# Optimization experiments

Hardware: AMD Instinct MI355X
Metric: run time of the kernel (lower is better)

Reference implementation:

```python
import jax, jax.numpy as jnp
import numpy as np

EMBED = 256
HEADS = 8
LEVELS = 1
POINTS = 4
HEAD_DIM = EMBED // HEADS  # 32
SPATIAL = [(200, 200)]     # static (H, W) per level
BS = 2
NQ = 40000
NV = sum(h * w for h, w in SPATIAL)


def setup_inputs() -> dict:
    key = jax.random.key(0)
    ks = jax.random.split(key, 12)
    s = 0.02
    inp = {
        "query": jax.random.normal(ks[0], (BS, NQ, EMBED), jnp.float32),
        "value": jax.random.normal(ks[1], (BS, NV, EMBED), jnp.float32),
        "reference_points": jax.random.uniform(ks[2], (BS, NQ, LEVELS, 2), jnp.float32),
        "spatial_shapes": jnp.array(SPATIAL, dtype=jnp.int32),
        "W_value": jax.random.normal(ks[3], (EMBED, EMBED), jnp.float32) * s,
        "b_value": jax.random.normal(ks[4], (EMBED,), jnp.float32) * s,
        "W_off": jax.random.normal(ks[5], (EMBED, HEADS * LEVELS * POINTS * 2), jnp.float32) * s,
        "b_off": jax.random.normal(ks[6], (HEADS * LEVELS * POINTS * 2,), jnp.float32) * s,
        "W_attn": jax.random.normal(ks[7], (EMBED, HEADS * LEVELS * POINTS), jnp.float32) * s,
        "b_attn": jax.random.normal(ks[8], (HEADS * LEVELS * POINTS,), jnp.float32) * s,
        "W_out": jax.random.normal(ks[9], (EMBED, EMBED), jnp.float32) * s,
        "b_out": jax.random.normal(ks[10], (EMBED,), jnp.float32) * s,
    }
    return inp


def _bilinear_sample(v_l, x, y, H, W):
    """grid_sample(bilinear, padding zeros, align_corners=False) on flat spatial.
    v_l: [bs, heads, H*W, d]; x, y: [bs, nq, heads, P] pixel coords.
    Returns [bs, nq, heads, P, d]."""
    bs = v_l.shape[0]
    nq = x.shape[1]
    x0 = jnp.floor(x)
    y0 = jnp.floor(y)
    out = jnp.zeros((bs, nq, HEADS, POINTS, HEAD_DIM), v_l.dtype)
    for dx in (0, 1):
        for dy in (0, 1):
            xi = x0 + dx
            yi = y0 + dy
            w = (1.0 - jnp.abs(x - xi)) * (1.0 - jnp.abs(y - yi))
            valid = (xi >= 0) & (xi <= W - 1) & (yi >= 0) & (yi <= H - 1)
            xi_c = jnp.clip(xi, 0, W - 1).astype(jnp.int32)
            yi_c = jnp.clip(yi, 0, H - 1).astype(jnp.int32)
            idx = yi_c * W + xi_c                               # [bs,nq,heads,P]
            idx = idx.transpose(0, 2, 1, 3).reshape(bs, HEADS, nq * POINTS)
            g = jnp.take_along_axis(v_l, idx[..., None], axis=2)  # [bs,heads,nq*P,d]
            g = g.reshape(bs, HEADS, nq, POINTS, HEAD_DIM).transpose(0, 2, 1, 3, 4)
            out = out + g * (w * valid.astype(w.dtype))[..., None]
    return out


def reference(query, value, reference_points, spatial_shapes,
              W_value, b_value, W_off, b_off, W_attn, b_attn, W_out, b_out):
    bs, nq, _ = query.shape
    # value projection
    v = (value @ W_value + b_value).reshape(bs, -1, HEADS, HEAD_DIM)
    v = v.transpose(0, 2, 1, 3)  # [bs, heads, nv, d]
    # sampling offsets and attention weights from query
    off = (query @ W_off + b_off).reshape(bs, nq, HEADS, LEVELS, POINTS, 2)
    aw = (query @ W_attn + b_attn).reshape(bs, nq, HEADS, LEVELS * POINTS)
    aw = jax.nn.softmax(aw, axis=-1).reshape(bs, nq, HEADS, LEVELS, POINTS)
    # sampling locations in [0,1] (reference_points last dim == 2 branch)
    normalizer = jnp.stack([spatial_shapes[:, 1], spatial_shapes[:, 0]], -1).astype(query.dtype)  # [L,2]=(W,H)
    loc = reference_points[:, :, None, :, None, :] + off / normalizer[None, None, None, :, None, :]
    out = jnp.zeros((bs, nq, HEADS, HEAD_DIM), query.dtype)
    start = 0
    for lvl, (H, W) in enumerate(SPATIAL):
        v_l = v[:, :, start:start + H * W]            # [bs,heads,HW,d]
        g = 2.0 * loc[:, :, :, lvl] - 1.0             # [bs,nq,heads,P,2] in [-1,1]
        px = ((g[..., 0] + 1.0) * W - 1.0) / 2.0      # align_corners=False
        py = ((g[..., 1] + 1.0) * H - 1.0) / 2.0
        sampled = _bilinear_sample(v_l, px, py, H, W)  # [bs,nq,heads,P,d]
        out = out + (sampled * aw[:, :, :, lvl, :, None]).sum(axis=3)
        start += H * W
    out = out.reshape(bs, nq, EMBED) @ W_out + b_out
    # dropout is identity in eval; identity residual = query (no query_pos)
    return out + query
```

## Files before the change

kernel.cpp:

```cpp
#include <hip/hip_runtime.h>


typedef float  f4  __attribute__((ext_vector_type(4)));
typedef float  fx4 __attribute__((ext_vector_type(4)));
typedef short  s8  __attribute__((ext_vector_type(8)));
typedef short  s4  __attribute__((ext_vector_type(4)));

#define KDIM    256
#define NVPIX   40000
#define GH      200
#define GW      200
#define LDP     68

__device__ __forceinline__ short f2bf(float f) {
  union { float f; unsigned u; } v; v.f = f;
  unsigned r = v.u + 0x7fffu + ((v.u >> 16) & 1u);
  return (short)(r >> 16);
}
__device__ __forceinline__ float bf2f(unsigned short h) {
  union { unsigned u; float f; } v; v.u = ((unsigned)h) << 16; return v.f;
}

__global__ void prep_k(const float* __restrict__ Wv, const float* __restrict__ Wo,
                       const float* __restrict__ Woff, const float* __restrict__ Wattn,
                       const float* __restrict__ boff, const float* __restrict__ battn,
                       unsigned short* __restrict__ Wv_t, unsigned short* __restrict__ Wo_t,
                       unsigned short* __restrict__ Wp_t, float* __restrict__ bp)
{
  int i = blockIdx.x * 256 + threadIdx.x;
  if (i < 65536) {
    int n = i >> 8, k = i & 255;
    Wv_t[i] = (unsigned short)f2bf(Wv[k * 256 + n]);
  } else if (i < 131072) {
    int j = i - 65536; int n = j >> 8, k = j & 255;
    Wo_t[j] = (unsigned short)f2bf(Wo[k * 256 + n]);
  } else if (i < 163840) {
    int j = i - 131072; int n = j >> 8, k = j & 255;
    float val = (n < 64) ? Woff[k * 64 + n] : ((n < 96) ? Wattn[k * 32 + (n - 64)] : 0.f);
    Wp_t[j] = (unsigned short)f2bf(val);
  } else if (i < 163968) {
    int j = i - 163840;
    bp[j] = (j < 64) ? boff[j] : ((j < 96) ? battn[j - 64] : 0.f);
  }
}

template<int ABF, int CBF, int RES>
__global__ __launch_bounds__(256)
void gemm_k(const void* __restrict__ Ap, const unsigned short* __restrict__ Bt,
            const float* __restrict__ bias, const float* __restrict__ resid,
            void* __restrict__ Cp, int N)
{
  __shared__ short As[128 * LDP];
  __shared__ short Bs[128 * LDP];
  const int t  = threadIdx.x;
  const int m0 = blockIdx.x * 128;
  const int n0 = blockIdx.y * 128;
  const int lane = t & 63;
  const int w  = t >> 6;
  const int wm = (w >> 1) * 64;
  const int wn = (w & 1) * 64;
  const int fr = lane & 15;
  const int quad = lane >> 4;

  fx4 acc[4][4];
  #pragma unroll
  for (int i = 0; i < 4; i++)
    #pragma unroll
    for (int j = 0; j < 4; j++) { fx4 z = {0.f, 0.f, 0.f, 0.f}; acc[i][j] = z; }

  f4 pa[8];
  s8 pa8[4];
  s8 pb[4];

  auto loadA = [&](int k0) {
    if (ABF) {
      const unsigned short* base = (const unsigned short*)Ap + (size_t)m0 * KDIM + k0;
      #pragma unroll
      for (int j = 0; j < 4; j++) {
        int id = t + j * 256;
        int row = id >> 3, kp = (id & 7) * 8;
        pa8[j] = *(const s8*)(base + (size_t)row * KDIM + kp);
      }
    } else {
      const float* base = (const float*)Ap + (size_t)m0 * KDIM + k0;
      #pragma unroll
      for (int j = 0; j < 8; j++) {
        int id = t + j * 256;
        int row = id >> 4, kp = (id & 15) * 4;
        pa[j] = *(const f4*)(base + (size_t)row * KDIM + kp);
      }
    }
  };
  auto loadB = [&](int k0) {
    const unsigned short* base = Bt + (size_t)n0 * KDIM + k0;
    #pragma unroll
    for (int j = 0; j < 4; j++) {
      int id = t + j * 256;
      int row = id >> 3, kp = (id & 7) * 8;
      pb[j] = *(const s8*)(base + (size_t)row * KDIM + kp);
    }
  };
  auto storeAB = [&]() {
    if (ABF) {
      #pragma unroll
      for (int j = 0; j < 4; j++) {
        int id = t + j * 256;
        int row = id >> 3, kp = (id & 7) * 8;
        *(s8*)(&As[row * LDP + kp]) = pa8[j];
      }
    } else {
      #pragma unroll
      for (int j = 0; j < 8; j++) {
        int id = t + j * 256;
        int row = id >> 4, kp = (id & 15) * 4;
        s4 c;
        #pragma unroll
        for (int e = 0; e < 4; e++) c[e] = f2bf(pa[j][e]);
        *(s4*)(&As[row * LDP + kp]) = c;
      }
    }
    #pragma unroll
    for (int j = 0; j < 4; j++) {
      int id = t + j * 256;
      int row = id >> 3, kp = (id & 7) * 8;
      *(s8*)(&Bs[row * LDP + kp]) = pb[j];
    }
  };

  loadA(0); loadB(0);
  #pragma unroll
  for (int it = 0; it < 4; ++it) {
    __syncthreads();
    storeAB();
    __syncthreads();
    if (it < 3) { loadA((it + 1) * 64); loadB((it + 1) * 64); }
    #pragma unroll
    for (int kk = 0; kk < 2; kk++) {
      s8 afr[4], bfr[4];
      #pragma unroll
      for (int i = 0; i < 4; i++)
        afr[i] = *(const s8*)(&As[(wm + i * 16 + fr) * LDP + kk * 32 + quad * 8]);
      #pragma unroll
      for (int i = 0; i < 4; i++)
        bfr[i] = *(const s8*)(&Bs[(wn + i * 16 + fr) * LDP + kk * 32 + quad * 8]);
      #pragma unroll
      for (int i = 0; i < 4; i++)
        #pragma unroll
        for (int j = 0; j < 4; j++)
          acc[i][j] = __builtin_amdgcn_mfma_f32_16x16x32_bf16(afr[i], bfr[j], acc[i][j], 0, 0, 0);
    }
  }

  #pragma unroll
  for (int i = 0; i < 4; i++) {
    const int mbase = m0 + wm + i * 16 + quad * 4;
    #pragma unroll
    for (int j = 0; j < 4; j++) {
      const int n = n0 + wn + j * 16 + fr;
      const float bn = bias[n];
      #pragma unroll
      for (int r = 0; r < 4; r++) {
        const size_t m = (size_t)(mbase + r);
        float v = acc[i][j][r] + bn;
        if (RES) v += resid[m * (size_t)N + n];
        if (CBF) ((unsigned short*)Cp)[m * (size_t)N + n] = (unsigned short)f2bf(v);
        else     ((float*)Cp)[m * (size_t)N + n] = v;
      }
    }
  }
}

__global__ __launch_bounds__(256)
void sample_k(const unsigned short* __restrict__ v, const float* __restrict__ p,
              const float* __restrict__ ref, unsigned short* __restrict__ o)
{
  const int t  = threadIdx.x;
  const int q0 = blockIdx.x * 8;
  __shared__ float sp[8][128];
  __shared__ float sref[16];
  {
    const float* pb = p + (size_t)q0 * 128;
    #pragma unroll
    for (int j = 0; j < 4; j++) {
      int i = t + j * 256;
      sp[i >> 7][i & 127] = pb[i];
    }
    if (t < 16) sref[t] = ref[(size_t)q0 * 2 + t];
  }
  __syncthreads();

  const int qi = t >> 5;
  const int h  = (t >> 2) & 7;
  const int dg = t & 3;
  const int q  = q0 + qi;
  const int b  = (q >= 40000) ? 1 : 0;

  const float lg0 = sp[qi][64 + h * 4 + 0], lg1 = sp[qi][64 + h * 4 + 1];
  const float lg2 = sp[qi][64 + h * 4 + 2], lg3 = sp[qi][64 + h * 4 + 3];
  const float mx = fmaxf(fmaxf(lg0, lg1), fmaxf(lg2, lg3));
  const float e0 = __expf(lg0 - mx), e1 = __expf(lg1 - mx);
  const float e2 = __expf(lg2 - mx), e3 = __expf(lg3 - mx);
  const float inv = 1.f / (e0 + e1 + e2 + e3);
  const float aws[4] = {e0 * inv, e1 * inv, e2 * inv, e3 * inv};
  const float rx = sref[qi * 2], ry = sref[qi * 2 + 1];

  const unsigned short* vb = v + (size_t)b * NVPIX * 256;
  const int cbase = h * 32 + dg * 8;

  float acc[8];
  #pragma unroll
  for (int e = 0; e < 8; e++) acc[e] = 0.f;

  #pragma unroll
  for (int pt = 0; pt < 4; ++pt) {
    const float ox = sp[qi][h * 8 + pt * 2], oy = sp[qi][h * 8 + pt * 2 + 1];
    const float px = rx * 200.f + ox - 0.5f;
    const float py = ry * 200.f + oy - 0.5f;
    const float x0f = floorf(px), y0f = floorf(py);
    const int ix = (int)x0f, iy = (int)y0f;
    const float fx = px - x0f, fy = py - y0f;
    const float a = aws[pt];
    const float vx0 = (ix >= 0 && ix < GW) ? 1.f : 0.f;
    const float vx1 = (ix + 1 >= 0 && ix + 1 < GW) ? 1.f : 0.f;
    const float vy0 = (iy >= 0 && iy < GH) ? 1.f : 0.f;
    const float vy1 = (iy + 1 >= 0 && iy + 1 < GH) ? 1.f : 0.f;
    const float w00 = a * (1.f - fx) * (1.f - fy) * vx0 * vy0;
    const float w01 = a * fx * (1.f - fy) * vx1 * vy0;
    const float w10 = a * (1.f - fx) * fy * vx0 * vy1;
    const float w11 = a * fx * fy * vx1 * vy1;
    const int ix0c = min(max(ix, 0), GW - 1);
    const int ix1c = min(max(ix + 1, 0), GW - 1);
    const int iy0c = min(max(iy, 0), GH - 1);
    const int iy1c = min(max(iy + 1, 0), GH - 1);
    const int r0 = iy0c * (GW * 256) + cbase;
    const int r1 = iy1c * (GW * 256) + cbase;
    s8 g00 = *(const s8*)(vb + r0 + ix0c * 256);
    s8 g01 = *(const s8*)(vb + r0 + ix1c * 256);
    s8 g10 = *(const s8*)(vb + r1 + ix0c * 256);
    s8 g11 = *(const s8*)(vb + r1 + ix1c * 256);
    #pragma unroll
    for (int e = 0; e < 8; e++) {
      acc[e] += w00 * bf2f((unsigned short)g00[e]) + w01 * bf2f((unsigned short)g01[e])
              + w10 * bf2f((unsigned short)g10[e]) + w11 * bf2f((unsigned short)g11[e]);
    }
  }

  s8 res;
  #pragma unroll
  for (int e = 0; e < 8; e++) res[e] = f2bf(acc[e]);
  *(s8*)(o + (size_t)q * 256 + cbase) = res;
}

extern "C" void kernel_launch(void* const* d_in, const int* in_sizes, int n_in,
                              void* d_out, int out_size, void* d_ws, size_t ws_size,
                              hipStream_t stream)
{
  const float* query = (const float*)d_in[0];
  const float* value = (const float*)d_in[1];
  const float* refp  = (const float*)d_in[2];
  const float* Wv    = (const float*)d_in[4];
  const float* bv    = (const float*)d_in[5];
  const float* Woff  = (const float*)d_in[6];
  const float* boff  = (const float*)d_in[7];
  const float* Wattn = (const float*)d_in[8];
  const float* battn = (const float*)d_in[9];
  const float* Wo    = (const float*)d_in[10];
  const float* bo    = (const float*)d_in[11];

  char* ws = (char*)d_ws;
  unsigned short* ws_v = (unsigned short*)ws;
  float*          ws_p = (float*)(ws + 40960000);
  unsigned short* ws_o = (unsigned short*)(ws + 81920000);
  unsigned short* Wv_t = (unsigned short*)(ws + 122880000);
  unsigned short* Wo_t = Wv_t + 65536;
  unsigned short* Wp_t = Wo_t + 65536;
  float*          bp   = (float*)(Wp_t + 32768);

  hipLaunchKernelGGL(prep_k, dim3(641), dim3(256), 0, stream,
                     Wv, Wo, Woff, Wattn, boff, battn, Wv_t, Wo_t, Wp_t, bp);
  hipLaunchKernelGGL((gemm_k<0, 1, 0>), dim3(625, 2), dim3(256), 0, stream,
                     (const void*)value, Wv_t, bv, (const float*)nullptr, (void*)ws_v, 256);
  hipLaunchKernelGGL((gemm_k<0, 0, 0>), dim3(625, 1), dim3(256), 0, stream,
                     (const void*)query, Wp_t, bp, (const float*)nullptr, (void*)ws_p, 128);
  hipLaunchKernelGGL(sample_k, dim3(10000), dim3(256), 0, stream,
                     ws_v, ws_p, refp, ws_o);
  hipLaunchKernelGGL((gemm_k<1, 0, 1>), dim3(625, 2), dim3(256), 0, stream,
                     (const void*)ws_o, Wo_t, bo, query, (void*)d_out, 256);
}
```

Measured before the change: 353.5 us.

## Fuse bilinear sampling with output projection GEMM and residual add

Merges the sampling kernel and the final output-projection GEMM into one kernel. Each block samples 64 queries (one thread per query-head computing all 32 channels) into shared memory in bf16, then runs an MFMA GEMM against Wo_t and adds bias plus the query residual. This removes the round trip of the sampled intermediate through global memory and one launch. In exchange each thread holds more registers (32 accumulators plus 16 MFMA accumulators), gathers are no longer spread across 4 threads per head, and only 1250 blocks are launched, which may lower occupancy and latency hiding.

```diff
diff --git a/kernel.cpp b/kernel.cpp
--- a/kernel.cpp
+++ b/kernel.cpp
@@ -11,6 +11,8 @@
 #define GH      200
 #define GW      200
 #define LDP     68
+#define SMPP    264
+#define BSP     36
 
 __device__ __forceinline__ short f2bf(float f) {
   union { float f; unsigned u; } v; v.f = f;
@@ -44,11 +46,10 @@
   }
 }
 
-template<int ABF, int CBF, int RES>
+template<int CBF>
 __global__ __launch_bounds__(256)
-void gemm_k(const void* __restrict__ Ap, const unsigned short* __restrict__ Bt,
-            const float* __restrict__ bias, const float* __restrict__ resid,
-            void* __restrict__ Cp, int N)
+void gemm_k(const float* __restrict__ Ap, const unsigned short* __restrict__ Bt,
+            const float* __restrict__ bias, void* __restrict__ Cp, int N)
 {
   __shared__ short As[128 * LDP];
   __shared__ short Bs[128 * LDP];
@@ -69,26 +70,15 @@
     for (int j = 0; j < 4; j++) { fx4 z = {0.f, 0.f, 0.f, 0.f}; acc[i][j] = z; }
 
   f4 pa[8];
-  s8 pa8[4];
   s8 pb[4];
 
   auto loadA = [&](int k0) {
-    if (ABF) {
-      const unsigned short* base = (const unsigned short*)Ap + (size_t)m0 * KDIM + k0;
-      #pragma unroll
-      for (int j = 0; j < 4; j++) {
-        int id = t + j * 256;
-        int row = id >> 3, kp = (id & 7) * 8;
-        pa8[j] = *(const s8*)(base + (size_t)row * KDIM + kp);
-      }
-    } else {
-      const float* base = (const float*)Ap + (size_t)m0 * KDIM + k0;
-      #pragma unroll
-      for (int j = 0; j < 8; j++) {
-        int id = t + j * 256;
-        int row = id >> 4, kp = (id & 15) * 4;
-        pa[j] = *(const f4*)(base + (size_t)row * KDIM + kp);
-      }
+    const float* base = Ap + (size_t)m0 * KDIM + k0;
+    #pragma unroll
+    for (int j = 0; j < 8; j++) {
+      int id = t + j * 256;
+      int row = id >> 4, kp = (id & 15) * 4;
+      pa[j] = *(const f4*)(base + (size_t)row * KDIM + kp);
     }
   };
   auto loadB = [&](int k0) {
@@ -101,23 +91,14 @@
     }
   };
   auto storeAB = [&]() {
-    if (ABF) {
-      #pragma unroll
-      for (int j = 0; j < 4; j++) {
-        int id = t + j * 256;
-        int row = id >> 3, kp = (id & 7) * 8;
-        *(s8*)(&As[row * LDP + kp]) = pa8[j];
-      }
-    } else {
-      #pragma unroll
-      for (int j = 0; j < 8; j++) {
-        int id = t + j * 256;
-        int row = id >> 4, kp = (id & 15) * 4;
-        s4 c;
-        #pragma unroll
-        for (int e = 0; e < 4; e++) c[e] = f2bf(pa[j][e]);
-        *(s4*)(&As[row * LDP + kp]) = c;
-      }
+    #pragma unroll
+    for (int j = 0; j < 8; j++) {
+      int id = t + j * 256;
+      int row = id >> 4, kp = (id & 15) * 4;
+      s4 c;
+      #pragma unroll
+      for (int e = 0; e < 4; e++) c[e] = f2bf(pa[j][e]);
+      *(s4*)(&As[row * LDP + kp]) = c;
     }
     #pragma unroll
     for (int j = 0; j < 4; j++) {
@@ -162,7 +143,6 @@
       for (int r = 0; r < 4; r++) {
         const size_t m = (size_t)(mbase + r);
         float v = acc[i][j][r] + bn;
-        if (RES) v += resid[m * (size_t)N + n];
         if (CBF) ((unsigned short*)Cp)[m * (size_t)N + n] = (unsigned short)f2bf(v);
         else     ((float*)Cp)[m * (size_t)N + n] = v;
       }
@@ -171,84 +151,143 @@
 }
 
 __global__ __launch_bounds__(256)
-void sample_k(const unsigned short* __restrict__ v, const float* __restrict__ p,
-              const float* __restrict__ ref, unsigned short* __restrict__ o)
+void fused_k(const unsigned short* __restrict__ v, const float* __restrict__ p,
+             const float* __restrict__ ref, const unsigned short* __restrict__ Wo_t,
+             const float* __restrict__ bo, const float* __restrict__ query,
+             float* __restrict__ out)
 {
+  __shared__ short smp[64 * SMPP];
+  __shared__ short Bs[256 * BSP];
   const int t  = threadIdx.x;
-  const int q0 = blockIdx.x * 8;
-  __shared__ float sp[8][128];
-  __shared__ float sref[16];
-  {
-    const float* pb = p + (size_t)q0 * 128;
-    #pragma unroll
-    for (int j = 0; j < 4; j++) {
-      int i = t + j * 256;
-      sp[i >> 7][i & 127] = pb[i];
-    }
-    if (t < 16) sref[t] = ref[(size_t)q0 * 2 + t];
-  }
-  __syncthreads();
-
-  const int qi = t >> 5;
-  const int h  = (t >> 2) & 7;
-  const int dg = t & 3;
-  const int q  = q0 + qi;
-  const int b  = (q >= 40000) ? 1 : 0;
-
-  const float lg0 = sp[qi][64 + h * 4 + 0], lg1 = sp[qi][64 + h * 4 + 1];
-  const float lg2 = sp[qi][64 + h * 4 + 2], lg3 = sp[qi][64 + h * 4 + 3];
-  const float mx = fmaxf(fmaxf(lg0, lg1), fmaxf(lg2, lg3));
-  const float e0 = __expf(lg0 - mx), e1 = __expf(lg1 - mx);
-  const float e2 = __expf(lg2 - mx), e3 = __expf(lg3 - mx);
-  const float inv = 1.f / (e0 + e1 + e2 + e3);
-  const float aws[4] = {e0 * inv, e1 * inv, e2 * inv, e3 * inv};
-  const float rx = sref[qi * 2], ry = sref[qi * 2 + 1];
-
-  const unsigned short* vb = v + (size_t)b * NVPIX * 256;
-  const int cbase = h * 32 + dg * 8;
-
-  float acc[8];
-  #pragma unroll
-  for (int e = 0; e < 8; e++) acc[e] = 0.f;
-
-  #pragma unroll
-  for (int pt = 0; pt < 4; ++pt) {
-    const float ox = sp[qi][h * 8 + pt * 2], oy = sp[qi][h * 8 + pt * 2 + 1];
-    const float px = rx * 200.f + ox - 0.5f;
-    const float py = ry * 200.f + oy - 0.5f;
-    const float x0f = floorf(px), y0f = floorf(py);
-    const int ix = (int)x0f, iy = (int)y0f;
-    const float fx = px - x0f, fy = py - y0f;
-    const float a = aws[pt];
-    const float vx0 = (ix >= 0 && ix < GW) ? 1.f : 0.f;
-    const float vx1 = (ix + 1 >= 0 && ix + 1 < GW) ? 1.f : 0.f;
-    const float vy0 = (iy >= 0 && iy < GH) ? 1.f : 0.f;
-    const float vy1 = (iy + 1 >= 0 && iy + 1 < GH) ? 1.f : 0.f;
-    const float w00 = a * (1.f - fx) * (1.f - fy) * vx0 * vy0;
-    const float w01 = a * fx * (1.f - fy) * vx1 * vy0;
-    const float w10 = a * (1.f - fx) * fy * vx0 * vy1;
-    const float w11 = a * fx * fy * vx1 * vy1;
-    const int ix0c = min(max(ix, 0), GW - 1);
-    const int ix1c = min(max(ix + 1, 0), GW - 1);
-    const int iy0c = min(max(iy, 0), GH - 1);
-    const int iy1c = min(max(iy + 1, 0), GH - 1);
-    const int r0 = iy0c * (GW * 256) + cbase;
-    const int r1 = iy1c * (GW * 256) + cbase;
-    s8 g00 = *(const s8*)(vb + r0 + ix0c * 256);
-    s8 g01 = *(const s8*)(vb + r0 + ix1c * 256);
-    s8 g10 = *(const s8*)(vb + r1 + ix0c * 256);
-    s8 g11 = *(const s8*)(vb + r1 + ix1c * 256);
-    #pragma unroll
-    for (int e = 0; e < 8; e++) {
-      acc[e] += w00 * bf2f((unsigned short)g00[e]) + w01 * bf2f((unsigned short)g01[e])
-              + w10 * bf2f((unsigned short)g10[e]) + w11 * bf2f((unsigned short)g11[e]);
-    }
-  }
-
-  s8 res;
-  #pragma unroll
-  for (int e = 0; e < 8; e++) res[e] = f2bf(acc[e]);
-  *(s8*)(o + (size_t)q * 256 + cbase) = res;
+  const int q0 = blockIdx.x * 64;
+
+  #pragma unroll
+  for (int itA = 0; itA < 2; ++itA) {
+    const int id = t + itA * 256;
+    const int qi = id >> 3;
+    const int h  = id & 7;
+    const int q  = q0 + qi;
+    const int b  = (q >= 40000) ? 1 : 0;
+    const float* pq = p + (size_t)q * 128;
+    const f4 off0 = *(const f4*)(pq + h * 8);
+    const f4 off1 = *(const f4*)(pq + h * 8 + 4);
+    const f4 lg   = *(const f4*)(pq + 64 + h * 4);
+    const float rx = ref[(size_t)q * 2], ry = ref[(size_t)q * 2 + 1];
+
+    const float mx = fmaxf(fmaxf(lg[0], lg[1]), fmaxf(lg[2], lg[3]));
+    const float e0 = __expf(lg[0] - mx), e1 = __expf(lg[1] - mx);
+    const float e2 = __expf(lg[2] - mx), e3 = __expf(lg[3] - mx);
+    const float inv = 1.f / (e0 + e1 + e2 + e3);
+    const float aws[4] = {e0 * inv, e1 * inv, e2 * inv, e3 * inv};
+    const float offs[8] = {off0[0], off0[1], off0[2], off0[3],
+                           off1[0], off1[1], off1[2], off1[3]};
+
+    const unsigned short* vb = v + (size_t)b * NVPIX * 256 + h * 32;
+
+    float acc[32];
+    #pragma unroll
+    for (int e = 0; e < 32; e++) acc[e] = 0.f;
+
+    #pragma unroll
+    for (int pt = 0; pt < 4; ++pt) {
+      const float px = rx * 200.f + offs[pt * 2]     - 0.5f;
+      const float py = ry * 200.f + offs[pt * 2 + 1] - 0.5f;
+      const float x0f = floorf(px), y0f = floorf(py);
+      const int ix = (int)x0f, iy = (int)y0f;
+      const float fx = px - x0f, fy = py - y0f;
+      const float a = aws[pt];
+      const float vx0 = (ix >= 0 && ix < GW) ? 1.f : 0.f;
+      const float vx1 = (ix + 1 >= 0 && ix + 1 < GW) ? 1.f : 0.f;
+      const float vy0 = (iy >= 0 && iy < GH) ? 1.f : 0.f;
+      const float vy1 = (iy + 1 >= 0 && iy + 1 < GH) ? 1.f : 0.f;
+      const float w00 = a * (1.f - fx) * (1.f - fy) * vx0 * vy0;
+      const float w01 = a * fx * (1.f - fy) * vx1 * vy0;
+      const float w10 = a * (1.f - fx) * fy * vx0 * vy1;
+      const float w11 = a * fx * fy * vx1 * vy1;
+      const int ix0c = min(max(ix, 0), GW - 1);
+      const int ix1c = min(max(ix + 1, 0), GW - 1);
+      const int iy0c = min(max(iy, 0), GH - 1);
+      const int iy1c = min(max(iy + 1, 0), GH - 1);
+      const unsigned short* c00 = vb + ((long)iy0c * GW + ix0c) * 256;
+      const unsigned short* c01 = vb + ((long)iy0c * GW + ix1c) * 256;
+      const unsigned short* c10 = vb + ((long)iy1c * GW + ix0c) * 256;
+      const unsigned short* c11 = vb + ((long)iy1c * GW + ix1c) * 256;
+      #pragma unroll
+      for (int g = 0; g < 4; g++) {
+        s8 g00 = *(const s8*)(c00 + g * 8);
+        s8 g01 = *(const s8*)(c01 + g * 8);
+        s8 g10 = *(const s8*)(c10 + g * 8);
+        s8 g11 = *(const s8*)(c11 + g * 8);
+        #pragma unroll
+        for (int e = 0; e < 8; e++) {
+          acc[g * 8 + e] += w00 * bf2f((unsigned short)g00[e])
+                          + w01 * bf2f((unsigned short)g01[e])
+                          + w10 * bf2f((unsigned short)g10[e])
+                          + w11 * bf2f((unsigned short)g11[e]);
+        }
+      }
+    }
+    #pragma unroll
+    for (int g = 0; g < 4; g++) {
+      s8 res;
+      #pragma unroll
+      for (int e = 0; e < 8; e++) res[e] = f2bf(acc[g * 8 + e]);
+      *(s8*)(&smp[qi * SMPP + h * 32 + g * 8]) = res;
+    }
+  }
+
+  const int lane = t & 63;
+  const int w    = t >> 6;
+  const int fr   = lane & 15;
+  const int quad = lane >> 4;
+
+  fx4 oacc[16];
+  #pragma unroll
+  for (int j = 0; j < 16; j++) { fx4 z = {0.f, 0.f, 0.f, 0.f}; oacc[j] = z; }
+
+  s8 pbB[4];
+  auto loadB = [&](int k0) {
+    #pragma unroll
+    for (int j = 0; j < 4; j++) {
+      int id = t + j * 256;
+      int row = id >> 2, kg = id & 3;
+      pbB[j] = *(const s8*)(Wo_t + (size_t)row * KDIM + k0 + kg * 8);
+    }
+  };
+  auto storeB = [&]() {
+    #pragma unroll
+    for (int j = 0; j < 4; j++) {
+      int id = t + j * 256;
+      int row = id >> 2, kg = id & 3;
+      *(s8*)(&Bs[row * BSP + kg * 8]) = pbB[j];
+    }
+  };
+
+  loadB(0);
+  #pragma unroll
+  for (int it = 0; it < 8; ++it) {
+    storeB();
+    __syncthreads();
+    if (it < 7) loadB((it + 1) * 32);
+    const s8 afr = *(const s8*)(&smp[(w * 16 + fr) * SMPP + it * 32 + quad * 8]);
+    #pragma unroll
+    for (int j = 0; j < 16; j++) {
+      const s8 bfr = *(const s8*)(&Bs[(j * 16 + fr) * BSP + quad * 8]);
+      oacc[j] = __builtin_amdgcn_mfma_f32_16x16x32_bf16(afr, bfr, oacc[j], 0, 0, 0);
+    }
+    if (it < 7) __syncthreads();
+  }
+
+  #pragma unroll
+  for (int j = 0; j < 16; j++) {
+    const int n = j * 16 + fr;
+    const float bn = bo[n];
+    #pragma unroll
+    for (int r = 0; r < 4; r++) {
+      const size_t m = (size_t)(q0 + w * 16 + quad * 4 + r);
+      out[m * 256 + n] = oacc[j][r] + bn + query[m * 256 + n];
+    }
+  }
 }
 
 extern "C" void kernel_launch(void* const* d_in, const int* in_sizes, int n_in,
@@ -270,7 +309,6 @@
   char* ws = (char*)d_ws;
   unsigned short* ws_v = (unsigned short*)ws;
   float*          ws_p = (float*)(ws + 40960000);
-  unsigned short* ws_o = (unsigned short*)(ws + 81920000);
   unsigned short* Wv_t = (unsigned short*)(ws + 122880000);
   unsigned short* Wo_t = Wv_t + 65536;
   unsigned short* Wp_t = Wo_t + 65536;
@@ -278,12 +316,10 @@
 
   hipLaunchKernelGGL(prep_k, dim3(641), dim3(256), 0, stream,
                      Wv, Wo, Woff, Wattn, boff, battn, Wv_t, Wo_t, Wp_t, bp);
-  hipLaunchKernelGGL((gemm_k<0, 1, 0>), dim3(625, 2), dim3(256), 0, stream,
-                     (const void*)value, Wv_t, bv, (const float*)nullptr, (void*)ws_v, 256);
-  hipLaunchKernelGGL((gemm_k<0, 0, 0>), dim3(625, 1), dim3(256), 0, stream,
-                     (const void*)query, Wp_t, bp, (const float*)nullptr, (void*)ws_p, 128);
-  hipLaunchKernelGGL(sample_k, dim3(10000), dim3(256), 0, stream,
-                     ws_v, ws_p, refp, ws_o);
-  hipLaunchKernelGGL((gemm_k<1, 0, 1>), dim3(625, 2), dim3(256), 0, stream,
-                     (const void*)ws_o, Wo_t, bo, query, (void*)d_out, 256);
-}
+  hipLaunchKernelGGL((gemm_k<1>), dim3(625, 2), dim3(256), 0, stream,
+                     value, Wv_t, bv, (void*)ws_v, 256);
+  hipLaunchKernelGGL((gemm_k<0>), dim3(625, 1), dim3(256), 0, stream,
+                     query, Wp_t, bp, (void*)ws_p, 128);
+  hipLaunchKernelGGL(fused_k, dim3(1250), dim3(256), 0, stream,
+                     ws_v, ws_p, refp, Wo_t, bo, query, (float*)d_out);
+}
```

After: 431.6 us. +22.1%, slower.
